# Optimization experiments

Hardware: AMD Instinct MI355X
Metric: run time of the kernel (lower is better)

Reference implementation:

```python
import jax, jax.numpy as jnp
import numpy as np

B, T, C, H = 4, 2048, 1024, 16
D = C // H  # head_dim = 64
SCALE = D ** -0.5


def setup_inputs() -> dict:
    key = jax.random.key(0)
    ks = jax.random.split(key, 5)
    s = C ** -0.5
    return {
        "x": jax.random.normal(ks[0], (B, T, C), dtype=jnp.float32),
        "W_qkv": jax.random.normal(ks[1], (C, 3 * C), dtype=jnp.float32) * s,
        "b_qkv": jnp.zeros((3 * C,), dtype=jnp.float32),
        "W_out": jax.random.normal(ks[2], (C, C), dtype=jnp.float32) * s,
        "b_out": jnp.zeros((C,), dtype=jnp.float32),
    }


def reference(x, W_qkv, b_qkv, W_out, b_out):
    Bx, Tx, Cx = x.shape
    qkv = x @ W_qkv + b_qkv                      # [B,T,3C]
    qkv = qkv.reshape(Bx, Tx, 3, H, D)
    q, k, v = qkv[:, :, 0], qkv[:, :, 1], qkv[:, :, 2]  # [B,T,H,D]
    # scores [B,H,T,T]
    scores = jnp.einsum("bthd,bshd->bhts", q, k) * SCALE
    causal = jnp.tril(jnp.ones((Tx, Tx), dtype=bool))
    scores = jnp.where(causal[None, None], scores, -jnp.inf)
    probs = jax.nn.softmax(scores, axis=-1)
    out = jnp.einsum("bhts,bshd->bthd", probs, v).reshape(Bx, Tx, Cx)
    return out @ W_out + b_out
```

## Files before the change

kernel.cpp:

```cpp
#include <hip/hip_runtime.h>
#include <cstdint>
#include <cstddef>

#define B_ 4
#define T_ 2048
#define C_ 1024
#define H_ 16
#define D_ 64
#define SCALE_ 0.125f

typedef _Float16 f16;
typedef f16 f16x4 __attribute__((ext_vector_type(4)));
typedef f16 f16x8 __attribute__((ext_vector_type(8)));
typedef float f32x4 __attribute__((ext_vector_type(4)));

__device__ __forceinline__ void async_ld16(const void* g, void* l) {
  __builtin_amdgcn_global_load_lds(
      (const __attribute__((address_space(1))) void*)g,
      (__attribute__((address_space(3))) void*)l,
      16, 0, 0);
}

__global__ void k_prep(const float* __restrict__ x, f16* __restrict__ xh,
                       const float* __restrict__ Wqkv, f16* __restrict__ WqkvT,
                       const float* __restrict__ Wout, f16* __restrict__ WoutT)
{
  __shared__ float tile[32][33];
  const int bx = blockIdx.x, t = threadIdx.x;
  if (bx < 8192) {
    int i = bx * 256 + t;
    float4 v = ((const float4*)x)[i];
    f16x4 h;
    h.x = (f16)v.x; h.y = (f16)v.y; h.z = (f16)v.z; h.w = (f16)v.w;
    ((f16x4*)xh)[i] = h;
    return;
  }
  const float* in; f16* out; int K, N, nt, kt;
  if (bx < 8192 + 3072) {
    int idx = bx - 8192; in = Wqkv; out = WqkvT; K = 1024; N = 3072;
    nt = idx % 96; kt = idx / 96;
  } else {
    int idx = bx - 11264; in = Wout; out = WoutT; K = 1024; N = 1024;
    nt = idx % 32; kt = idx / 32;
  }
  int tx = t & 31, ty = t >> 5;
  int k0 = kt * 32, n0 = nt * 32;
#pragma unroll
  for (int i = 0; i < 32; i += 8)
    tile[ty + i][tx] = in[(size_t)(k0 + ty + i) * N + n0 + tx];
  __syncthreads();
#pragma unroll
  for (int i = 0; i < 32; i += 8)
    out[(size_t)(n0 + ty + i) * K + k0 + tx] = (f16)tile[tx][ty + i];
}

__global__ __launch_bounds__(256, 3)
void k_gemm256(const f16* __restrict__ A, const f16* __restrict__ Bt,
               const float* __restrict__ bias, f16* __restrict__ Ch,
               f16* __restrict__ VtOut, int M, int N, int K)
{
  __shared__ __align__(16) f16 As[2][256 * 32];
  __shared__ __align__(16) f16 Bs[2][128 * 32];
  const int t = threadIdx.x;
  const int wave = t >> 6, lane = t & 63, lr = lane & 15, quad = lane >> 4;
  const int row0 = blockIdx.y * 256, col0 = blockIdx.x * 128;
  const int wm = (wave >> 1) * 128, wn = (wave & 1) * 64;

  f32x4 acc[8][4] = {};

  const int sw = ((t & 3) ^ ((t >> 4) & 3)) * 8;
  const f16* gA = A + (size_t)(row0 + (t >> 2)) * K + sw;
  const f16* gB = Bt + (size_t)(col0 + (t >> 2)) * K + sw;
  const size_t rowskip = (size_t)64 * K;
  const int rc = (quad ^ (lr >> 2)) * 8;

  {
    f16* lA = As[0] + wave * 512;
    f16* lB = Bs[0] + wave * 512;
    async_ld16(gA,                lA);
    async_ld16(gA + rowskip,      lA + 2048);
    async_ld16(gA + 2 * rowskip,  lA + 4096);
    async_ld16(gA + 3 * rowskip,  lA + 6144);
    async_ld16(gB,                lB);
    async_ld16(gB + rowskip,      lB + 2048);
  }

  const int iters = K >> 5;
  for (int it = 0; it < iters; ++it) {
    __syncthreads();
    const int buf = it & 1;
    if (it + 1 < iters) {
      const int k0 = (it + 1) * 32;
      f16* lA = As[buf ^ 1] + wave * 512;
      f16* lB = Bs[buf ^ 1] + wave * 512;
      async_ld16(gA + k0,               lA);
      async_ld16(gA + rowskip + k0,     lA + 2048);
      async_ld16(gA + 2 * rowskip + k0, lA + 4096);
      async_ld16(gA + 3 * rowskip + k0, lA + 6144);
      async_ld16(gB + k0,               lB);
      async_ld16(gB + rowskip + k0,     lB + 2048);
    }
    const f16* As_ = As[buf];
    const f16* Bs_ = Bs[buf];

    f16x8 bf[4];
#pragma unroll
    for (int i = 0; i < 4; ++i)
      bf[i] = *(const f16x8*)&Bs_[(wn + i * 16 + lr) * 32 + rc];
#pragma unroll
    for (int mi = 0; mi < 8; ++mi) {
      f16x8 af = *(const f16x8*)&As_[(wm + mi * 16 + lr) * 32 + rc];
#pragma unroll
      for (int ni = 0; ni < 4; ++ni)
        acc[mi][ni] = __builtin_amdgcn_mfma_f32_16x16x32_f16(af, bf[ni], acc[mi][ni], 0, 0, 0);
    }
  }

  if (VtOut != nullptr && col0 >= 2048) {
#pragma unroll
    for (int ni = 0; ni < 4; ++ni) {
      const int cb = col0 + wn + ni * 16 - 2048;
      const int h = cb >> 6;
      const int dd = (cb & 63) + lr;
      const float bv = bias[2048 + cb + lr];
#pragma unroll
      for (int mi = 0; mi < 8; ++mi) {
#pragma unroll
        for (int r = 0; r < 4; ++r) {
          const int row = row0 + wm + mi * 16 + quad * 4 + r;
          const int bb = row >> 11, tt = row & 2047;
          VtOut[((size_t)(bb * 16 + h) * 64 + dd) * T_ + tt] = (f16)(acc[mi][ni][r] + bv);
        }
      }
    }
  } else {
#pragma unroll
    for (int mi = 0; mi < 8; ++mi) {
#pragma unroll
      for (int ni = 0; ni < 4; ++ni) {
        int col = col0 + wn + ni * 16 + lr;
        float bv = bias[col];
#pragma unroll
        for (int r = 0; r < 4; ++r) {
          int row = row0 + wm + mi * 16 + quad * 4 + r;
          Ch[(size_t)row * N + col] = (f16)(acc[mi][ni][r] + bv);
        }
      }
    }
  }
}

__global__ __launch_bounds__(256, 3)
void k_gemm_bt(const f16* __restrict__ A, const f16* __restrict__ Bt,
               const float* __restrict__ bias, float* __restrict__ Cf,
               int M, int N, int K)
{
  __shared__ __align__(16) f16 As[2][128 * 32];
  __shared__ __align__(16) f16 Bs[2][128 * 32];
  const int t = threadIdx.x;
  const int wave = t >> 6, lane = t & 63, lr = lane & 15, quad = lane >> 4;
  const int row0 = blockIdx.y * 128, col0 = blockIdx.x * 128;
  const int wm = (wave >> 1) * 64, wn = (wave & 1) * 64;

  f32x4 acc[4][4] = {};

  const int sw = ((t & 3) ^ ((t >> 4) & 3)) * 8;
  const f16* gA = A + (size_t)(row0 + (t >> 2)) * K + sw;
  const f16* gB = Bt + (size_t)(col0 + (t >> 2)) * K + sw;
  const size_t rowskip = (size_t)64 * K;
  const int rc = (quad ^ (lr >> 2)) * 8;

  {
    f16* lA = As[0] + wave * 512;
    f16* lB = Bs[0] + wave * 512;
    async_ld16(gA,           lA);
    async_ld16(gA + rowskip, lA + 2048);
    async_ld16(gB,           lB);
    async_ld16(gB + rowskip, lB + 2048);
  }

  const int iters = K >> 5;
  for (int it = 0; it < iters; ++it) {
    __syncthreads();
    const int buf = it & 1;
    if (it + 1 < iters) {
      const int k0 = (it + 1) * 32;
      f16* lA = As[buf ^ 1] + wave * 512;
      f16* lB = Bs[buf ^ 1] + wave * 512;
      async_ld16(gA + k0,           lA);
      async_ld16(gA + rowskip + k0, lA + 2048);
      async_ld16(gB + k0,           lB);
      async_ld16(gB + rowskip + k0, lB + 2048);
    }
    const f16* As_ = As[buf];
    const f16* Bs_ = Bs[buf];

    f16x8 af[4], bf[4];
#pragma unroll
    for (int i = 0; i < 4; ++i) {
      af[i] = *(const f16x8*)&As_[(wm + i * 16 + lr) * 32 + rc];
      bf[i] = *(const f16x8*)&Bs_[(wn + i * 16 + lr) * 32 + rc];
    }
#pragma unroll
    for (int mi = 0; mi < 4; ++mi)
#pragma unroll
      for (int ni = 0; ni < 4; ++ni)
        acc[mi][ni] = __builtin_amdgcn_mfma_f32_16x16x32_f16(af[mi], bf[ni], acc[mi][ni], 0, 0, 0);
  }

#pragma unroll
  for (int mi = 0; mi < 4; ++mi) {
#pragma unroll
    for (int ni = 0; ni < 4; ++ni) {
      int col = col0 + wn + ni * 16 + lr;
      float bv = bias[col];
#pragma unroll
      for (int r = 0; r < 4; ++r) {
        int row = row0 + wm + mi * 16 + quad * 4 + r;
        Cf[(size_t)row * N + col] = acc[mi][ni][r] + bv;
      }
    }
  }
}

__global__ __launch_bounds__(256, 4)
void k_flash(const f16* __restrict__ QKV, const f16* __restrict__ Vt, f16* __restrict__ O)
{
  __shared__ __align__(16) f16 Ks[2][64 * 64];
  __shared__ __align__(16) f16 Vs[2][64 * 64];
  __shared__ __align__(16) f16 Ps[4][16 * 64];

  const int a = blockIdx.x, bh = blockIdx.y;
  const int b = bh >> 4, h = bh & 15;
  const int qtA = a, qtB = 31 - a;
  const int t = threadIdx.x, wave = t >> 6, lane = t & 63, lr = lane & 15, quad = lane >> 4;
  const int lr3 = lr & 7;
  const int c0 = quad ^ lr3;
  const int c1 = c0 ^ 4;

  const f16 scl = (f16)0.125f;
  const f16* qpA = QKV + (size_t)(b * T_ + qtA * 64 + wave * 16 + lr) * 3072 + h * 64;
  const f16* qpB = QKV + (size_t)(b * T_ + qtB * 64 + wave * 16 + lr) * 3072 + h * 64;
  f16x8 qA0 = *(const f16x8*)(qpA + quad * 8)      * scl;
  f16x8 qA1 = *(const f16x8*)(qpA + 32 + quad * 8) * scl;
  f16x8 qB0 = *(const f16x8*)(qpB + quad * 8)      * scl;
  f16x8 qB1 = *(const f16x8*)(qpB + 32 + quad * 8) * scl;

  float lA_[4] = {0.f, 0.f, 0.f, 0.f};
  float lB_[4] = {0.f, 0.f, 0.f, 0.f};
  f32x4 oA[4] = {}, oB[4] = {};

  const int sw = ((t & 7) ^ ((t >> 3) & 7)) * 8;
  const f16* gK = QKV + (size_t)(b * T_ + (t >> 3)) * 3072 + 1024 + h * 64 + sw;
  const f16* gV = Vt + ((size_t)bh * 64 + (t >> 3)) * T_ + sw;

  f16* myP = Ps[wave];
  f16* pw0 = myP + (quad * 4) * 64 + ((0 ^ quad) << 4) + lr;
  f16* pw1 = myP + (quad * 4) * 64 + ((1 ^ quad) << 4) + lr;
  f16* pw2 = myP + (quad * 4) * 64 + ((2 ^ quad) << 4) + lr;
  f16* pw3 = myP + (quad * 4) * 64 + ((3 ^ quad) << 4) + lr;
  const f16* pr0 = myP + lr * 64 + ((((quad >> 1))     ^ (lr >> 2)) << 4) + ((quad & 1) << 3);
  const f16* pr1 = myP + lr * 64 + ((((quad >> 1) ^ 2) ^ (lr >> 2)) << 4) + ((quad & 1) << 3);

  const int last = qtB;

  {
    f16* lK = Ks[0] + wave * 512;
    f16* lV = Vs[0] + wave * 512;
    async_ld16(gK,                     lK);
    async_ld16(gK + (size_t)32 * 3072, lK + 2048);
    async_ld16(gV,                     lV);
    async_ld16(gV + (size_t)32 * T_,   lV + 2048);
  }

  for (int kt = 0; kt <= last; ++kt) {
    __syncthreads();
    const int buf = kt & 1;
    if (kt < last) {
      const f16* gk = gK + (size_t)((kt + 1) * 64) * 3072;
      const f16* gv = gV + (kt + 1) * 64;
      f16* lK = Ks[buf ^ 1] + wave * 512;
      f16* lV = Vs[buf ^ 1] + wave * 512;
      async_ld16(gk,                     lK);
      async_ld16(gk + (size_t)32 * 3072, lK + 2048);
      async_ld16(gv,                     lV);
      async_ld16(gv + (size_t)32 * T_,   lV + 2048);
    }
    const f16* K_ = Ks[buf];
    const f16* V_ = Vs[buf];
    const bool actA = (kt <= qtA);

    {
      f32x4 s4[4];
#pragma unroll
      for (int ni = 0; ni < 4; ++ni) {
        const f16* kr = K_ + (ni * 16 + lr) * 64;
        f16x8 k0 = *(const f16x8*)(kr + c0 * 8);
        f16x8 k1 = *(const f16x8*)(kr + c1 * 8);
        f32x4 z = {};
        z = __builtin_amdgcn_mfma_f32_16x16x32_f16(qB0, k0, z, 0, 0, 0);
        z = __builtin_amdgcn_mfma_f32_16x16x32_f16(qB1, k1, z, 0, 0, 0);
        s4[ni] = z;
      }
      if (kt == qtB) {
        const int rloc = wave * 16 + quad * 4;
#pragma unroll
        for (int r = 0; r < 4; ++r) {
#pragma unroll
          for (int ni = 0; ni < 4; ++ni)
            if (ni * 16 + lr > rloc + r) s4[ni][r] = -1e30f;
        }
      }
#pragma unroll
      for (int r = 0; r < 4; ++r) {
        float e0 = __expf(s4[0][r]), e1 = __expf(s4[1][r]);
        float e2 = __expf(s4[2][r]), e3 = __expf(s4[3][r]);
        lB_[r] += (e0 + e1) + (e2 + e3);
        pw0[r * 64] = (f16)e0; pw1[r * 64] = (f16)e1;
        pw2[r * 64] = (f16)e2; pw3[r * 64] = (f16)e3;
      }
      f16x8 pB0 = *(const f16x8*)pr0;
      f16x8 pB1 = *(const f16x8*)pr1;
#pragma unroll
      for (int ni = 0; ni < 4; ++ni) {
        const f16* vr = V_ + (ni * 16 + lr) * 64;
        f16x8 v0 = *(const f16x8*)(vr + c0 * 8);
        f16x8 v1 = *(const f16x8*)(vr + c1 * 8);
        oB[ni] = __builtin_amdgcn_mfma_f32_16x16x32_f16(pB0, v0, oB[ni], 0, 0, 0);
        oB[ni] = __builtin_amdgcn_mfma_f32_16x16x32_f16(pB1, v1, oB[ni], 0, 0, 0);
      }
    }

    if (actA) {
      f32x4 s4[4];
#pragma unroll
      for (int ni = 0; ni < 4; ++ni) {
        const f16* kr = K_ + (ni * 16 + lr) * 64;
        f16x8 k0 = *(const f16x8*)(kr + c0 * 8);
        f16x8 k1 = *(const f16x8*)(kr + c1 * 8);
        f32x4 z = {};
        z = __builtin_amdgcn_mfma_f32_16x16x32_f16(qA0, k0, z, 0, 0, 0);
        z = __builtin_amdgcn_mfma_f32_16x16x32_f16(qA1, k1, z, 0, 0, 0);
        s4[ni] = z;
      }
      if (kt == qtA) {
        const int rloc = wave * 16 + quad * 4;
#pragma unroll
        for (int r = 0; r < 4; ++r) {
#pragma unroll
          for (int ni = 0; ni < 4; ++ni)
            if (ni * 16 + lr > rloc + r) s4[ni][r] = -1e30f;
        }
      }
#pragma unroll
      for (int r = 0; r < 4; ++r) {
        float e0 = __expf(s4[0][r]), e1 = __expf(s4[1][r]);
        float e2 = __expf(s4[2][r]), e3 = __expf(s4[3][r]);
        lA_[r] += (e0 + e1) + (e2 + e3);
        pw0[r * 64] = (f16)e0; pw1[r * 64] = (f16)e1;
        pw2[r * 64] = (f16)e2; pw3[r * 64] = (f16)e3;
      }
      f16x8 pA0 = *(const f16x8*)pr0;
      f16x8 pA1 = *(const f16x8*)pr1;
#pragma unroll
      for (int ni = 0; ni < 4; ++ni) {
        const f16* vr = V_ + (ni * 16 + lr) * 64;
        f16x8 v0 = *(const f16x8*)(vr + c0 * 8);
        f16x8 v1 = *(const f16x8*)(vr + c1 * 8);
        oA[ni] = __builtin_amdgcn_mfma_f32_16x16x32_f16(pA0, v0, oA[ni], 0, 0, 0);
        oA[ni] = __builtin_amdgcn_mfma_f32_16x16x32_f16(pA1, v1, oA[ni], 0, 0, 0);
      }
    }
  }

#pragma unroll
  for (int r = 0; r < 4; ++r) {
    float la = lA_[r], lb = lB_[r];
#pragma unroll
    for (int off = 1; off < 16; off <<= 1) {
      la += __shfl_xor(la, off, 64);
      lb += __shfl_xor(lb, off, 64);
    }
    const int rowA = qtA * 64 + wave * 16 + quad * 4 + r;
    const int rowB = qtB * 64 + wave * 16 + quad * 4 + r;
    float invA = 1.f / la;
    float invB = 1.f / lb;
#pragma unroll
    for (int ni = 0; ni < 4; ++ni) {
      O[(size_t)(b * T_ + rowA) * C_ + h * 64 + ni * 16 + lr] = (f16)(oA[ni][r] * invA);
      O[(size_t)(b * T_ + rowB) * C_ + h * 64 + ni * 16 + lr] = (f16)(oB[ni][r] * invB);
    }
  }
}

extern "C" void kernel_launch(void* const* d_in, const int* in_sizes, int n_in,
                              void* d_out, int out_size, void* d_ws, size_t ws_size,
                              hipStream_t stream)
{
  const float* x    = (const float*)d_in[0];
  const float* Wqkv = (const float*)d_in[1];
  const float* bqkv = (const float*)d_in[2];
  const float* Wout = (const float*)d_in[3];
  const float* bout = (const float*)d_in[4];
  float* out = (float*)d_out;

  f16* xh    = (f16*)d_ws;
  f16* WqkvT = xh + (size_t)8192 * 1024;
  f16* WoutT = WqkvT + (size_t)3072 * 1024;
  f16* QKV   = WoutT + (size_t)1024 * 1024;
  f16* VtG   = QKV + (size_t)8192 * 3072;
  f16* Oh    = VtG + (size_t)64 * 64 * 2048;

  k_prep<<<12288, 256, 0, stream>>>(x, xh, Wqkv, WqkvT, Wout, WoutT);

  k_gemm256<<<dim3(3072 / 128, 8192 / 256), 256, 0, stream>>>(
      xh, WqkvT, bqkv, QKV, VtG, 8192, 3072, 1024);

  k_flash<<<dim3(16, B_ * H_), 256, 0, stream>>>(QKV, VtG, Oh);

  k_gemm_bt<<<dim3(1024 / 128, 8192 / 128), 256, 0, stream>>>(
      Oh, WoutT, bout, out, 8192, 1024, 1024);
}
```

Measured before the change: 261.8 us.

## Compute transposed scores to keep P in registers and reuse 256-row GEMM

The flash kernel now computes S^T as K·Q so the MFMA accumulator layout matches the B operand of a 16x16x16 PV MFMA. This removes the shared-memory round trip for P and the per-row shuffle reductions. The K fragment loads are shared between the A and B query tiles, and exp2 with log2e folded into the Q scale replaces __expf. The output projection now reuses the 256x128 GEMM kernel with an fp32 output path instead of the separate 128x128 kernel, which changes tile shape and occupancy.

```diff
diff --git a/kernel.cpp b/kernel.cpp
--- a/kernel.cpp
+++ b/kernel.cpp
@@ -7,7 +7,6 @@
 #define C_ 1024
 #define H_ 16
 #define D_ 64
-#define SCALE_ 0.125f
 
 typedef _Float16 f16;
 typedef f16 f16x4 __attribute__((ext_vector_type(4)));
@@ -57,7 +56,8 @@
 __global__ __launch_bounds__(256, 3)
 void k_gemm256(const f16* __restrict__ A, const f16* __restrict__ Bt,
                const float* __restrict__ bias, f16* __restrict__ Ch,
-               f16* __restrict__ VtOut, int M, int N, int K)
+               float* __restrict__ Cf, f16* __restrict__ VtOut,
+               int M, int N, int K)
 {
   __shared__ __align__(16) f16 As[2][256 * 32];
   __shared__ __align__(16) f16 Bs[2][128 * 32];
@@ -133,7 +133,7 @@
         }
       }
     }
-  } else {
+  } else if (Ch != nullptr) {
 #pragma unroll
     for (int mi = 0; mi < 8; ++mi) {
 #pragma unroll
@@ -147,77 +147,18 @@
         }
       }
     }
-  }
-}
-
-__global__ __launch_bounds__(256, 3)
-void k_gemm_bt(const f16* __restrict__ A, const f16* __restrict__ Bt,
-               const float* __restrict__ bias, float* __restrict__ Cf,
-               int M, int N, int K)
-{
-  __shared__ __align__(16) f16 As[2][128 * 32];
-  __shared__ __align__(16) f16 Bs[2][128 * 32];
-  const int t = threadIdx.x;
-  const int wave = t >> 6, lane = t & 63, lr = lane & 15, quad = lane >> 4;
-  const int row0 = blockIdx.y * 128, col0 = blockIdx.x * 128;
-  const int wm = (wave >> 1) * 64, wn = (wave & 1) * 64;
-
-  f32x4 acc[4][4] = {};
-
-  const int sw = ((t & 3) ^ ((t >> 4) & 3)) * 8;
-  const f16* gA = A + (size_t)(row0 + (t >> 2)) * K + sw;
-  const f16* gB = Bt + (size_t)(col0 + (t >> 2)) * K + sw;
-  const size_t rowskip = (size_t)64 * K;
-  const int rc = (quad ^ (lr >> 2)) * 8;
-
-  {
-    f16* lA = As[0] + wave * 512;
-    f16* lB = Bs[0] + wave * 512;
-    async_ld16(gA,           lA);
-    async_ld16(gA + rowskip, lA + 2048);
-    async_ld16(gB,           lB);
-    async_ld16(gB + rowskip, lB + 2048);
-  }
-
-  const int iters = K >> 5;
-  for (int it = 0; it < iters; ++it) {
-    __syncthreads();
-    const int buf = it & 1;
-    if (it + 1 < iters) {
-      const int k0 = (it + 1) * 32;
-      f16* lA = As[buf ^ 1] + wave * 512;
-      f16* lB = Bs[buf ^ 1] + wave * 512;
-      async_ld16(gA + k0,           lA);
-      async_ld16(gA + rowskip + k0, lA + 2048);
-      async_ld16(gB + k0,           lB);
-      async_ld16(gB + rowskip + k0, lB + 2048);
-    }
-    const f16* As_ = As[buf];
-    const f16* Bs_ = Bs[buf];
-
-    f16x8 af[4], bf[4];
-#pragma unroll
-    for (int i = 0; i < 4; ++i) {
-      af[i] = *(const f16x8*)&As_[(wm + i * 16 + lr) * 32 + rc];
-      bf[i] = *(const f16x8*)&Bs_[(wn + i * 16 + lr) * 32 + rc];
-    }
-#pragma unroll
-    for (int mi = 0; mi < 4; ++mi)
-#pragma unroll
-      for (int ni = 0; ni < 4; ++ni)
-        acc[mi][ni] = __builtin_amdgcn_mfma_f32_16x16x32_f16(af[mi], bf[ni], acc[mi][ni], 0, 0, 0);
-  }
-
-#pragma unroll
-  for (int mi = 0; mi < 4; ++mi) {
-#pragma unroll
-    for (int ni = 0; ni < 4; ++ni) {
-      int col = col0 + wn + ni * 16 + lr;
-      float bv = bias[col];
-#pragma unroll
-      for (int r = 0; r < 4; ++r) {
-        int row = row0 + wm + mi * 16 + quad * 4 + r;
-        Cf[(size_t)row * N + col] = acc[mi][ni][r] + bv;
+  } else {
+#pragma unroll
+    for (int mi = 0; mi < 8; ++mi) {
+#pragma unroll
+      for (int ni = 0; ni < 4; ++ni) {
+        int col = col0 + wn + ni * 16 + lr;
+        float bv = bias[col];
+#pragma unroll
+        for (int r = 0; r < 4; ++r) {
+          int row = row0 + wm + mi * 16 + quad * 4 + r;
+          Cf[(size_t)row * N + col] = acc[mi][ni][r] + bv;
+        }
       }
     }
   }
@@ -228,7 +169,6 @@
 {
   __shared__ __align__(16) f16 Ks[2][64 * 64];
   __shared__ __align__(16) f16 Vs[2][64 * 64];
-  __shared__ __align__(16) f16 Ps[4][16 * 64];
 
   const int a = blockIdx.x, bh = blockIdx.y;
   const int b = bh >> 4, h = bh & 15;
@@ -238,7 +178,7 @@
   const int c0 = quad ^ lr3;
   const int c1 = c0 ^ 4;
 
-  const f16 scl = (f16)0.125f;
+  const f16 scl = (f16)0.18033688f;
   const f16* qpA = QKV + (size_t)(b * T_ + qtA * 64 + wave * 16 + lr) * 3072 + h * 64;
   const f16* qpB = QKV + (size_t)(b * T_ + qtB * 64 + wave * 16 + lr) * 3072 + h * 64;
   f16x8 qA0 = *(const f16x8*)(qpA + quad * 8)      * scl;
@@ -246,21 +186,18 @@
   f16x8 qB0 = *(const f16x8*)(qpB + quad * 8)      * scl;
   f16x8 qB1 = *(const f16x8*)(qpB + 32 + quad * 8) * scl;
 
-  float lA_[4] = {0.f, 0.f, 0.f, 0.f};
-  float lB_[4] = {0.f, 0.f, 0.f, 0.f};
+  float lA = 0.f, lB = 0.f;
   f32x4 oA[4] = {}, oB[4] = {};
 
   const int sw = ((t & 7) ^ ((t >> 3) & 7)) * 8;
   const f16* gK = QKV + (size_t)(b * T_ + (t >> 3)) * 3072 + 1024 + h * 64 + sw;
   const f16* gV = Vt + ((size_t)bh * 64 + (t >> 3)) * T_ + sw;
 
-  f16* myP = Ps[wave];
-  f16* pw0 = myP + (quad * 4) * 64 + ((0 ^ quad) << 4) + lr;
-  f16* pw1 = myP + (quad * 4) * 64 + ((1 ^ quad) << 4) + lr;
-  f16* pw2 = myP + (quad * 4) * 64 + ((2 ^ quad) << 4) + lr;
-  f16* pw3 = myP + (quad * 4) * 64 + ((3 ^ quad) << 4) + lr;
-  const f16* pr0 = myP + lr * 64 + ((((quad >> 1))     ^ (lr >> 2)) << 4) + ((quad & 1) << 3);
-  const f16* pr1 = myP + lr * 64 + ((((quad >> 1) ^ 2) ^ (lr >> 2)) << 4) + ((quad & 1) << 3);
+  const int vbase = lr * 64 + (quad & 1) * 4;
+  int voff[4];
+#pragma unroll
+  for (int kc = 0; kc < 4; ++kc)
+    voff[kc] = (((2 * kc + (quad >> 1)) ^ lr3) << 3);
 
   const int last = qtB;
 
@@ -290,106 +227,95 @@
     const f16* V_ = Vs[buf];
     const bool actA = (kt <= qtA);
 
-    {
-      f32x4 s4[4];
-#pragma unroll
-      for (int ni = 0; ni < 4; ++ni) {
-        const f16* kr = K_ + (ni * 16 + lr) * 64;
-        f16x8 k0 = *(const f16x8*)(kr + c0 * 8);
-        f16x8 k1 = *(const f16x8*)(kr + c1 * 8);
-        f32x4 z = {};
-        z = __builtin_amdgcn_mfma_f32_16x16x32_f16(qB0, k0, z, 0, 0, 0);
-        z = __builtin_amdgcn_mfma_f32_16x16x32_f16(qB1, k1, z, 0, 0, 0);
-        s4[ni] = z;
-      }
-      if (kt == qtB) {
-        const int rloc = wave * 16 + quad * 4;
+    f32x4 sB[4], sA[4];
+#pragma unroll
+    for (int mt = 0; mt < 4; ++mt) {
+      const f16* kr = K_ + (mt * 16 + lr) * 64;
+      f16x8 k0 = *(const f16x8*)(kr + c0 * 8);
+      f16x8 k1 = *(const f16x8*)(kr + c1 * 8);
+      f32x4 z = {};
+      z = __builtin_amdgcn_mfma_f32_16x16x32_f16(k0, qB0, z, 0, 0, 0);
+      z = __builtin_amdgcn_mfma_f32_16x16x32_f16(k1, qB1, z, 0, 0, 0);
+      sB[mt] = z;
+      if (actA) {
+        f32x4 y = {};
+        y = __builtin_amdgcn_mfma_f32_16x16x32_f16(k0, qA0, y, 0, 0, 0);
+        y = __builtin_amdgcn_mfma_f32_16x16x32_f16(k1, qA1, y, 0, 0, 0);
+        sA[mt] = y;
+      }
+    }
+
+    const int qloc = wave * 16 + lr;
+    if (kt == qtB) {
+#pragma unroll
+      for (int mt = 0; mt < 4; ++mt)
+#pragma unroll
+        for (int r = 0; r < 4; ++r)
+          if (mt * 16 + quad * 4 + r > qloc) sB[mt][r] = -1e30f;
+    }
+    if (kt == qtA) {
+#pragma unroll
+      for (int mt = 0; mt < 4; ++mt)
+#pragma unroll
+        for (int r = 0; r < 4; ++r)
+          if (mt * 16 + quad * 4 + r > qloc) sA[mt][r] = -1e30f;
+    }
+
+    f16x4 pB[4], pA[4];
+#pragma unroll
+    for (int mt = 0; mt < 4; ++mt) {
+#pragma unroll
+      for (int r = 0; r < 4; ++r) {
+        float e = exp2f(sB[mt][r]);
+        lB += e;
+        pB[mt][r] = (f16)e;
+      }
+    }
+    if (actA) {
+#pragma unroll
+      for (int mt = 0; mt < 4; ++mt) {
 #pragma unroll
         for (int r = 0; r < 4; ++r) {
-#pragma unroll
-          for (int ni = 0; ni < 4; ++ni)
-            if (ni * 16 + lr > rloc + r) s4[ni][r] = -1e30f;
+          float e = exp2f(sA[mt][r]);
+          lA += e;
+          pA[mt][r] = (f16)e;
         }
       }
-#pragma unroll
-      for (int r = 0; r < 4; ++r) {
-        float e0 = __expf(s4[0][r]), e1 = __expf(s4[1][r]);
-        float e2 = __expf(s4[2][r]), e3 = __expf(s4[3][r]);
-        lB_[r] += (e0 + e1) + (e2 + e3);
-        pw0[r * 64] = (f16)e0; pw1[r * 64] = (f16)e1;
-        pw2[r * 64] = (f16)e2; pw3[r * 64] = (f16)e3;
-      }
-      f16x8 pB0 = *(const f16x8*)pr0;
-      f16x8 pB1 = *(const f16x8*)pr1;
-#pragma unroll
-      for (int ni = 0; ni < 4; ++ni) {
-        const f16* vr = V_ + (ni * 16 + lr) * 64;
-        f16x8 v0 = *(const f16x8*)(vr + c0 * 8);
-        f16x8 v1 = *(const f16x8*)(vr + c1 * 8);
-        oB[ni] = __builtin_amdgcn_mfma_f32_16x16x32_f16(pB0, v0, oB[ni], 0, 0, 0);
-        oB[ni] = __builtin_amdgcn_mfma_f32_16x16x32_f16(pB1, v1, oB[ni], 0, 0, 0);
-      }
-    }
-
-    if (actA) {
-      f32x4 s4[4];
-#pragma unroll
-      for (int ni = 0; ni < 4; ++ni) {
-        const f16* kr = K_ + (ni * 16 + lr) * 64;
-        f16x8 k0 = *(const f16x8*)(kr + c0 * 8);
-        f16x8 k1 = *(const f16x8*)(kr + c1 * 8);
-        f32x4 z = {};
-        z = __builtin_amdgcn_mfma_f32_16x16x32_f16(qA0, k0, z, 0, 0, 0);
-        z = __builtin_amdgcn_mfma_f32_16x16x32_f16(qA1, k1, z, 0, 0, 0);
-        s4[ni] = z;
-      }
-      if (kt == qtA) {
-        const int rloc = wave * 16 + quad * 4;
-#pragma unroll
-        for (int r = 0; r < 4; ++r) {
-#pragma unroll
-          for (int ni = 0; ni < 4; ++ni)
-            if (ni * 16 + lr > rloc + r) s4[ni][r] = -1e30f;
-        }
-      }
-#pragma unroll
-      for (int r = 0; r < 4; ++r) {
-        float e0 = __expf(s4[0][r]), e1 = __expf(s4[1][r]);
-        float e2 = __expf(s4[2][r]), e3 = __expf(s4[3][r]);
-        lA_[r] += (e0 + e1) + (e2 + e3);
-        pw0[r * 64] = (f16)e0; pw1[r * 64] = (f16)e1;
-        pw2[r * 64] = (f16)e2; pw3[r * 64] = (f16)e3;
-      }
-      f16x8 pA0 = *(const f16x8*)pr0;
-      f16x8 pA1 = *(const f16x8*)pr1;
-#pragma unroll
-      for (int ni = 0; ni < 4; ++ni) {
-        const f16* vr = V_ + (ni * 16 + lr) * 64;
-        f16x8 v0 = *(const f16x8*)(vr + c0 * 8);
-        f16x8 v1 = *(const f16x8*)(vr + c1 * 8);
-        oA[ni] = __builtin_amdgcn_mfma_f32_16x16x32_f16(pA0, v0, oA[ni], 0, 0, 0);
-        oA[ni] = __builtin_amdgcn_mfma_f32_16x16x32_f16(pA1, v1, oA[ni], 0, 0, 0);
-      }
-    }
-  }
-
-#pragma unroll
-  for (int r = 0; r < 4; ++r) {
-    float la = lA_[r], lb = lB_[r];
-#pragma unroll
-    for (int off = 1; off < 16; off <<= 1) {
-      la += __shfl_xor(la, off, 64);
-      lb += __shfl_xor(lb, off, 64);
-    }
-    const int rowA = qtA * 64 + wave * 16 + quad * 4 + r;
-    const int rowB = qtB * 64 + wave * 16 + quad * 4 + r;
-    float invA = 1.f / la;
-    float invB = 1.f / lb;
-#pragma unroll
-    for (int ni = 0; ni < 4; ++ni) {
-      O[(size_t)(b * T_ + rowA) * C_ + h * 64 + ni * 16 + lr] = (f16)(oA[ni][r] * invA);
-      O[(size_t)(b * T_ + rowB) * C_ + h * 64 + ni * 16 + lr] = (f16)(oB[ni][r] * invB);
-    }
+    }
+
+#pragma unroll
+    for (int dt = 0; dt < 4; ++dt) {
+      const f16* vb = V_ + dt * 1024 + vbase;
+#pragma unroll
+      for (int kc = 0; kc < 4; ++kc) {
+        f16x4 va = *(const f16x4*)(vb + voff[kc]);
+        oB[dt] = __builtin_amdgcn_mfma_f32_16x16x16f16(va, pB[kc], oB[dt], 0, 0, 0);
+        if (actA)
+          oA[dt] = __builtin_amdgcn_mfma_f32_16x16x16f16(va, pA[kc], oA[dt], 0, 0, 0);
+      }
+    }
+  }
+
+  lA += __shfl_xor(lA, 16, 64);
+  lA += __shfl_xor(lA, 32, 64);
+  lB += __shfl_xor(lB, 16, 64);
+  lB += __shfl_xor(lB, 32, 64);
+  const float invA = 1.f / lA;
+  const float invB = 1.f / lB;
+  const int rowA = qtA * 64 + wave * 16 + lr;
+  const int rowB = qtB * 64 + wave * 16 + lr;
+  f16* oAp = O + (size_t)(b * T_ + rowA) * C_ + h * 64 + quad * 4;
+  f16* oBp = O + (size_t)(b * T_ + rowB) * C_ + h * 64 + quad * 4;
+#pragma unroll
+  for (int dt = 0; dt < 4; ++dt) {
+    f16x4 ha, hb;
+#pragma unroll
+    for (int r = 0; r < 4; ++r) {
+      ha[r] = (f16)(oA[dt][r] * invA);
+      hb[r] = (f16)(oB[dt][r] * invB);
+    }
+    *(f16x4*)(oAp + dt * 16) = ha;
+    *(f16x4*)(oBp + dt * 16) = hb;
   }
 }
 
@@ -414,10 +340,10 @@
   k_prep<<<12288, 256, 0, stream>>>(x, xh, Wqkv, WqkvT, Wout, WoutT);
 
   k_gemm256<<<dim3(3072 / 128, 8192 / 256), 256, 0, stream>>>(
-      xh, WqkvT, bqkv, QKV, VtG, 8192, 3072, 1024);
+      xh, WqkvT, bqkv, QKV, nullptr, VtG, 8192, 3072, 1024);
 
   k_flash<<<dim3(16, B_ * H_), 256, 0, stream>>>(QKV, VtG, Oh);
 
-  k_gemm_bt<<<dim3(1024 / 128, 8192 / 128), 256, 0, stream>>>(
-      Oh, WoutT, bout, out, 8192, 1024, 1024);
-}
+  k_gemm256<<<dim3(1024 / 128, 8192 / 256), 256, 0, stream>>>(
+      Oh, WoutT, bout, nullptr, out, nullptr, 8192, 1024, 1024);
+}
```

After: 280.2 us. +7.0%, slower.
